# Performance work log

Measured on AMD Instinct MI355X. Metric: run time of the kernel, lower is better.

Reference implementation:

```python
import jax, jax.numpy as jnp
import numpy as np

ASPECT_RATIOS = jnp.array([0.5, 1.0, 2.0], dtype=jnp.float32)
SCALES = jnp.array([1.0, 2.0, 4.0, 8.0, 16.0], dtype=jnp.float32)
BASE_SIZE = 16
STRIDE = 16
NEG_OVERLAP = 0.3
POS_OVERLAP = 0.7
PADDING = 0.0
RPN_BATCH = 256
RPN_FG_FRACTION = 0.5


def _mkanchors(ws, hs, x_ctr, y_ctr):
    return jnp.stack([x_ctr - 0.5 * (ws - 1), y_ctr - 0.5 * (hs - 1),
                      x_ctr + 0.5 * (ws - 1), y_ctr + 0.5 * (hs - 1)], axis=-1)


def _base_anchors():
    w = h = float(BASE_SIZE)
    x_ctr = y_ctr = 0.5 * (BASE_SIZE - 1)
    size = w * h
    size_ratios = size / ASPECT_RATIOS
    ws = jnp.round(jnp.sqrt(size_ratios))
    hs = jnp.round(ws * ASPECT_RATIOS)
    ratio_anchors = _mkanchors(ws, hs, x_ctr, y_ctr)          # (R,4)
    rw = ratio_anchors[:, 2] - ratio_anchors[:, 0] + 1
    rh = ratio_anchors[:, 3] - ratio_anchors[:, 1] + 1
    rx = ratio_anchors[:, 0] + 0.5 * (rw - 1)
    ry = ratio_anchors[:, 1] + 0.5 * (rh - 1)
    ws2 = rw[:, None] * SCALES[None, :]                        # (R,S)
    hs2 = rh[:, None] * SCALES[None, :]
    anchors = _mkanchors(ws2, hs2, rx[:, None], ry[:, None])   # (R,S,4)
    return anchors.reshape(-1, 4)                              # (A=R*S,4)


def _shifted_anchors(r, c):
    base = _base_anchors()                                     # (A,4)
    sx = jnp.arange(c, dtype=jnp.float32) * STRIDE
    sy = jnp.arange(r, dtype=jnp.float32) * STRIDE
    SX, SY = jnp.meshgrid(sx, sy)                              # (r,c)
    shifts = jnp.stack([SX.ravel(), SY.ravel(), SX.ravel(), SY.ravel()], axis=1)
    return (shifts[:, None, :] + base[None, :, :]).reshape(-1, 4)  # (K=r*c*A,4)


def _iou(a, b):
    area_a = (a[:, 2] - a[:, 0] + 1) * (a[:, 3] - a[:, 1] + 1)
    area_b = (b[:, 2] - b[:, 0] + 1) * (b[:, 3] - b[:, 1] + 1)
    iw = jnp.minimum(a[:, None, 2], b[None, :, 2]) - jnp.maximum(a[:, None, 0], b[None, :, 0]) + 1
    ih = jnp.minimum(a[:, None, 3], b[None, :, 3]) - jnp.maximum(a[:, None, 1], b[None, :, 1]) + 1
    inter = jnp.maximum(iw, 0) * jnp.maximum(ih, 0)
    return inter / (area_a[:, None] + area_b[None, :] - inter)


def _bbox_transform(ex, gt):
    ew = ex[:, 2] - ex[:, 0] + 1.0
    eh = ex[:, 3] - ex[:, 1] + 1.0
    ecx = ex[:, 0] + 0.5 * ew
    ecy = ex[:, 1] + 0.5 * eh
    gw = gt[:, 2] - gt[:, 0] + 1.0
    gh = gt[:, 3] - gt[:, 1] + 1.0
    gcx = gt[:, 0] + 0.5 * gw
    gcy = gt[:, 1] + 0.5 * gh
    return jnp.stack([(gcx - ecx) / ew, (gcy - ecy) / eh,
                      jnp.log(gw / ew), jnp.log(gh / eh)], axis=1)


def reference(target_bounding_boxes, metadata, scores):
    meta = metadata[0]
    gt = target_bounding_boxes[0]                               # (G,4)
    r, c = scores.shape[1], scores.shape[2]
    anchors = _shifted_anchors(r, c)                            # (K,4)
    K = anchors.shape[0]
    h, w = meta[0], meta[1]

    # anchors fully inside the image (padding=0); outside anchors masked
    inside = ((anchors[:, 0] >= -PADDING) & (anchors[:, 1] >= -PADDING) &
              (anchors[:, 2] < w + PADDING) & (anchors[:, 3] < h + PADDING))

    clipped = jnp.stack([jnp.clip(anchors[:, 0], 0.0, w - 1),
                         jnp.clip(anchors[:, 1], 0.0, h - 1),
                         jnp.clip(anchors[:, 2], 0.0, w - 1),
                         jnp.clip(anchors[:, 3], 0.0, h - 1)], axis=1)

    overlaps = _iou(clipped, gt)                                # (K,G)
    overlaps = jnp.where(inside[:, None], overlaps, -1.0)       # ignore outside anchors
    argmax_overlaps = jnp.argmax(overlaps, axis=1)              # best gt per anchor
    max_overlaps = jnp.max(overlaps, axis=1)
    gt_argmax = jnp.argmax(overlaps, axis=0)                    # best anchor per gt

    labels = jnp.full((K,), -1.0, dtype=jnp.float32)
    labels = jnp.where(inside & (max_overlaps < NEG_OVERLAP), 0.0, labels)
    labels = labels.at[gt_argmax].set(1.0)                      # dedup handled by .set
    labels = jnp.where(inside & (max_overlaps >= POS_OVERLAP), 1.0, labels)
    labels = jnp.where(inside, labels, -1.0)                    # unmap fill=-1

    # deterministic subsampling (original shuffles randomly): keep first-by-index
    num_fg = int(RPN_FG_FRACTION * RPN_BATCH)
    pos = labels == 1.0
    pos_rank = jnp.cumsum(pos.astype(jnp.int32))
    labels = jnp.where(pos & (pos_rank > num_fg), -1.0, labels)
    num_pos = jnp.minimum(pos.sum(), num_fg)
    num_bg = RPN_BATCH - num_pos
    neg = labels == 0.0
    neg_rank = jnp.cumsum(neg.astype(jnp.int32))
    labels = jnp.where(neg & (neg_rank > num_bg), -1.0, labels)

    matched_gt = gt[argmax_overlaps]                            # (K,4) gather
    bbox_targets = _bbox_transform(clipped, matched_gt)
    bbox_targets = jnp.where(inside[:, None], bbox_targets, 0.0)  # unmap fill=0

    return anchors[None], bbox_targets[None], labels[None]


def setup_inputs() -> dict:
    key = jax.random.key(0)
    k1, k2 = jax.random.split(key)
    H = W = 1600
    G = 100
    r = c = H // STRIDE                                          # 100
    A = 15                                                       # 3 ratios * 5 scales
    xy = jax.random.uniform(k1, (G, 2), minval=0.0, maxval=1400.0)
    wh = jax.random.uniform(k2, (G, 2), minval=16.0, maxval=200.0)
    gt = jnp.concatenate([xy, xy + wh], axis=1)[None]            # (1,G,4)
    metadata = jnp.array([[float(H), float(W), 1.0]], dtype=jnp.float32)
    scores = jnp.zeros((1, r, c, A), dtype=jnp.float32)          # only shape is used
    return {"target_bounding_boxes": gt, "metadata": metadata, "scores": scores}
```

## Files before the change

### kernel.cpp

```cpp
#include <hip/hip_runtime.h>
#include <math.h>


#define NUM_A 15
#define NUM_FG 128
#define RPN_BATCH 256
#define BLOCK 256
#define MAXG 256
#define MAXNB 1024

#define EXT_X1 (-176.f)
#define EXT_X2 (191.f)
#define EXT_Y1 (-168.f)
#define EXT_Y2 (183.f)

__device__ __forceinline__ void base_anchor(int a, float& bx1, float& by1,
                                            float& bx2, float& by2) {
    const float RW[3] = {23.f, 16.f, 11.f};
    const float RH[3] = {12.f, 16.f, 22.f};
    int i = a / 5;
    int j = a - i * 5;
    float sc = (float)(1 << j);
    float w = RW[i] * sc;
    float h = RH[i] * sc;
    bx1 = 7.5f - 0.5f * (w - 1.f);
    by1 = 7.5f - 0.5f * (h - 1.f);
    bx2 = 7.5f + 0.5f * (w - 1.f);
    by2 = 7.5f + 0.5f * (h - 1.f);
}

__device__ __forceinline__ void anchor_coords(int k, int c, float& x1, float& y1,
                                              float& x2, float& y2) {
    int a = k % NUM_A;
    int p = k / NUM_A;
    int xi = p % c;
    int yi = p / c;
    float bx1, by1, bx2, by2;
    base_anchor(a, bx1, by1, bx2, by2);
    float sx = (float)xi * 16.f;
    float sy = (float)yi * 16.f;
    x1 = sx + bx1;  y1 = sy + by1;
    x2 = sx + bx2;  y2 = sy + by2;
}

__device__ __forceinline__ unsigned long long packvk(float v, int k) {
    unsigned u = __float_as_uint(v);
    u = (u & 0x80000000u) ? ~u : (u | 0x80000000u);
    return ((unsigned long long)u << 32) | (unsigned)(~k);
}

__global__ void __launch_bounds__(BLOCK) k_main(
        const float* __restrict__ gt, const float* __restrict__ meta,
        float* __restrict__ out_anch, float* __restrict__ out_bb,
        float* __restrict__ lab0, int* __restrict__ posc, int* __restrict__ negc,
        unsigned long long* __restrict__ bestg, int K, int c, int G) {
    __shared__ float4 s_gt[MAXG];
    __shared__ float4 s_gtc[MAXG];
    __shared__ int s_gidx[MAXG];
    __shared__ unsigned long long s_best[MAXG];
    __shared__ int s_nl;
    __shared__ int swp[4], swn[4];
    int tid = threadIdx.x;
    int lane = tid & 63, wid = tid >> 6;
    const float4* gtv = (const float4*)gt;

    float h = meta[0], w = meta[1];
    float wm1 = __fsub_rn(w, 1.f), hm1 = __fsub_rn(h, 1.f);

    int k0 = blockIdx.x * BLOCK;
    int k1 = min(k0 + BLOCK - 1, K - 1);
    int p0 = k0 / NUM_A, p1 = k1 / NUM_A;
    int y0 = p0 / c, y1 = p1 / c;
    int xm0, xm1;
    if (y0 == y1) { xm0 = p0 - y0 * c; xm1 = p1 - y1 * c; }
    else          { xm0 = 0;           xm1 = c - 1; }
    float bbx1 = fminf(fmaxf((float)(xm0 * 16) + EXT_X1, 0.f), wm1);
    float bbx2 = fminf(fmaxf((float)(xm1 * 16) + EXT_X2, 0.f), wm1);
    float bby1 = fminf(fmaxf((float)(y0 * 16) + EXT_Y1, 0.f), hm1);
    float bby2 = fminf(fmaxf((float)(y1 * 16) + EXT_Y2, 0.f), hm1);

    if (tid == 0) s_nl = 0;
    for (int g = tid; g < G; g += BLOCK) s_best[g] = 0ULL;
    __syncthreads();
    for (int g = tid; g < G; g += BLOCK) {
        float4 gb = gtv[g];
        s_gt[g] = gb;
        float ox = __fadd_rn(__fsub_rn(fminf(bbx2, gb.z), fmaxf(bbx1, gb.x)), 1.f);
        float oy = __fadd_rn(__fsub_rn(fminf(bby2, gb.w), fmaxf(bby1, gb.y)), 1.f);
        if (ox > 0.f && oy > 0.f) {
            int slot = atomicAdd(&s_nl, 1);
            s_gtc[slot] = gb;
            s_gidx[slot] = g;
        }
    }
    __syncthreads();
    int NL = s_nl;

    int k = blockIdx.x * BLOCK + tid;
    bool valid = (k < K);

    float x1, y1f, x2, y2f;
    anchor_coords(k, c, x1, y1f, x2, y2f);
    if (valid) ((float4*)out_anch)[k] = make_float4(x1, y1f, x2, y2f);
    bool inside = (x1 >= 0.f) && (y1f >= 0.f) && (x2 < w) && (y2f < h);
    bool act_anchor = valid && inside;

    float cx1 = fminf(fmaxf(x1, 0.f), wm1);
    float cy1 = fminf(fmaxf(y1f, 0.f), hm1);
    float cx2 = fminf(fmaxf(x2, 0.f), wm1);
    float cy2 = fminf(fmaxf(y2f, 0.f), hm1);
    float area_a = __fmul_rn(__fadd_rn(__fsub_rn(cx2, cx1), 1.f),
                             __fadd_rn(__fsub_rn(cy2, cy1), 1.f));

    float maxv = 0.f;
    int arg = 0;
    if (act_anchor) {
        for (int i = 0; i < NL; ++i) {
            float4 gb = s_gtc[i];
            int g = s_gidx[i];
            float gw = __fadd_rn(__fsub_rn(gb.z, gb.x), 1.f);
            float gh = __fadd_rn(__fsub_rn(gb.w, gb.y), 1.f);
            float areab = __fmul_rn(gw, gh);
            float iw = __fadd_rn(__fsub_rn(fminf(cx2, gb.z), fmaxf(cx1, gb.x)), 1.f);
            float ih = __fadd_rn(__fsub_rn(fminf(cy2, gb.w), fmaxf(cy1, gb.y)), 1.f);
            float inter = __fmul_rn(fmaxf(iw, 0.f), fmaxf(ih, 0.f));
            if (inter > 0.f) {
                float denom = __fsub_rn(__fadd_rn(area_a, areab), inter);
                float v = __fdiv_rn(inter, denom);
                atomicMax(&s_best[g], packvk(v, k));
                if (v > maxv || (v == maxv && g < arg)) { maxv = v; arg = g; }
            }
        }
    }
    __syncthreads();
    for (int g = tid; g < G; g += BLOCK)
        if (s_best[g] != 0ULL) atomicMax(&bestg[g], s_best[g]);

    float labf = -1.f;
    if (valid) {
        float t0 = 0.f, t1 = 0.f, t2 = 0.f, t3 = 0.f;
        if (inside) {
            labf = (maxv >= 0.7f) ? 1.f : (maxv < 0.3f ? 0.f : -1.f);
            float4 gb = s_gt[arg];
            float ew  = __fadd_rn(__fsub_rn(cx2, cx1), 1.f);
            float eh  = __fadd_rn(__fsub_rn(cy2, cy1), 1.f);
            float ecx = __fadd_rn(cx1, __fmul_rn(0.5f, ew));
            float ecy = __fadd_rn(cy1, __fmul_rn(0.5f, eh));
            float gw  = __fadd_rn(__fsub_rn(gb.z, gb.x), 1.f);
            float gh  = __fadd_rn(__fsub_rn(gb.w, gb.y), 1.f);
            float gcx = __fadd_rn(gb.x, __fmul_rn(0.5f, gw));
            float gcy = __fadd_rn(gb.y, __fmul_rn(0.5f, gh));
            t0 = __fdiv_rn(__fsub_rn(gcx, ecx), ew);
            t1 = __fdiv_rn(__fsub_rn(gcy, ecy), eh);
            t2 = logf(__fdiv_rn(gw, ew));
            t3 = logf(__fdiv_rn(gh, eh));
        }
        ((float4*)out_bb)[k] = make_float4(t0, t1, t2, t3);
        lab0[k] = labf;
    }

    bool pos = valid && (labf == 1.f);
    bool neg = valid && (labf == 0.f);
    unsigned long long bp = __ballot(pos ? 1 : 0);
    unsigned long long bn = __ballot(neg ? 1 : 0);
    if (lane == 0) { swp[wid] = __popcll(bp); swn[wid] = __popcll(bn); }
    __syncthreads();
    if (tid == 0) {
        posc[blockIdx.x] = swp[0] + swp[1] + swp[2] + swp[3];
        negc[blockIdx.x] = swn[0] + swn[1] + swn[2] + swn[3];
    }
}

__global__ void __launch_bounds__(BLOCK) k_finish(
        const float* __restrict__ lab0, float* __restrict__ out_lab,
        const int* __restrict__ posc, const int* __restrict__ negc,
        const unsigned long long* __restrict__ bestg, int K, int NB, int G) {
    __shared__ int s_p[MAXNB], s_n[MAXNB];
    __shared__ int s_cp[BLOCK], s_cn[BLOCK];
    __shared__ int s_k[MAXG];
    __shared__ unsigned char s_over[BLOCK];
    __shared__ int swp[4], swn[4];
    int tid = threadIdx.x;
    int lane = tid & 63, wid = tid >> 6;
    int base = tid * 4;

    int4 pv = ((const int4*)posc)[tid];
    int4 nv = ((const int4*)negc)[tid];
    if (base + 0 >= NB) pv.x = 0;  if (base + 1 >= NB) pv.y = 0;
    if (base + 2 >= NB) pv.z = 0;  if (base + 3 >= NB) pv.w = 0;
    if (base + 0 >= NB) nv.x = 0;  if (base + 1 >= NB) nv.y = 0;
    if (base + 2 >= NB) nv.z = 0;  if (base + 3 >= NB) nv.w = 0;
    ((int4*)s_p)[tid] = pv;
    ((int4*)s_n)[tid] = nv;

    s_over[tid] = 0;
    int kstar = -1;
    if (tid < G) {
        unsigned long long u = bestg[tid];
        if (u != 0ULL)
            kstar = (int)(~(unsigned)(u & 0xffffffffu));
    }
    if (tid < MAXG) s_k[tid] = kstar;
    __syncthreads();
    bool mine = (kstar >= 0);
    if (mine) {
        for (int j = 0; j < tid; ++j)
            if (s_k[j] == kstar) { mine = false; break; }
    }
    if (mine) {
        int b = kstar / BLOCK;
        float oldl = lab0[kstar];
        if (oldl != 1.f) {
            atomicAdd(&s_p[b], 1);
            if (oldl == 0.f) atomicAdd(&s_n[b], -1);
        }
        if (b == (int)blockIdx.x) s_over[kstar - b * BLOCK] = 1;
    }
    __syncthreads();

    int p0 = s_p[base], p1 = s_p[base + 1], p2 = s_p[base + 2], p3 = s_p[base + 3];
    int n0 = s_n[base], n1 = s_n[base + 1], n2 = s_n[base + 2], n3 = s_n[base + 3];
    int sump = p0 + p1 + p2 + p3, sumn = n0 + n1 + n2 + n3;
    s_cp[tid] = sump; s_cn[tid] = sumn;
    __syncthreads();
    int vp = sump, vn = sumn;
    for (int off = 1; off < BLOCK; off <<= 1) {
        int ap = 0, an = 0;
        if (tid >= off) { ap = s_cp[tid - off]; an = s_cn[tid - off]; }
        __syncthreads();
        vp += ap; vn += an;
        s_cp[tid] = vp; s_cn[tid] = vn;
        __syncthreads();
    }
    int ep = vp - sump, en = vn - sumn;
    s_p[base] = ep; ep += p0; s_p[base + 1] = ep; ep += p1;
    s_p[base + 2] = ep; ep += p2; s_p[base + 3] = ep;
    s_n[base] = en; en += n0; s_n[base + 1] = en; en += n1;
    s_n[base + 2] = en; en += n2; s_n[base + 3] = en;
    __syncthreads();
    int total_pos = s_cp[BLOCK - 1];
    int np = total_pos < NUM_FG ? total_pos : NUM_FG;
    int nbg = RPN_BATCH - np;

    int k = blockIdx.x * BLOCK + tid;
    bool valid = (k < K);
    float lv = -1.f;
    if (valid) lv = s_over[tid] ? 1.f : lab0[k];
    bool posf = valid && (lv == 1.f);
    bool negf = valid && (lv == 0.f);
    unsigned long long lm = (1ULL << lane) - 1ULL;
    unsigned long long bp2 = __ballot(posf ? 1 : 0);
    unsigned long long bn2 = __ballot(negf ? 1 : 0);
    if (lane == 0) { swp[wid] = __popcll(bp2); swn[wid] = __popcll(bn2); }
    __syncthreads();
    int poff = 0, noff = 0;
    for (int wv = 0; wv < wid; ++wv) { poff += swp[wv]; noff += swn[wv]; }
    int prank = s_p[blockIdx.x] + poff + __popcll(bp2 & lm) + 1;
    int nrank = s_n[blockIdx.x] + noff + __popcll(bn2 & lm) + 1;
    if (valid) {
        float outv = lv;
        if (posf && prank > NUM_FG) outv = -1.f;
        if (negf && nrank > nbg)    outv = -1.f;
        out_lab[k] = outv;
    }
}

extern "C" void kernel_launch(void* const* d_in, const int* in_sizes, int n_in,
                              void* d_out, int out_size, void* d_ws, size_t ws_size,
                              hipStream_t stream) {
    const float* gt   = (const float*)d_in[0];
    const float* meta = (const float*)d_in[1];
    int G  = in_sizes[0] / 4;
    int rc = in_sizes[2] / NUM_A;
    int c = 1;
    while ((long long)(c + 1) * (c + 1) <= (long long)rc) ++c;
    int K  = rc * NUM_A;
    int NB = (K + BLOCK - 1) / BLOCK;

    float* out      = (float*)d_out;
    float* out_anch = out;
    float* out_bb   = out + (size_t)4 * K;
    float* out_lab  = out + (size_t)8 * K;

    unsigned long long* bestg = (unsigned long long*)d_ws;
    int* posc  = (int*)(bestg + MAXG);
    int* negc  = posc + MAXNB;
    float* lab0 = (float*)(negc + MAXNB);

    hipMemsetAsync(bestg, 0, MAXG * sizeof(unsigned long long), stream);
    hipLaunchKernelGGL(k_main, dim3(NB), dim3(BLOCK), 0, stream,
                       gt, meta, out_anch, out_bb, lab0, posc, negc, bestg, K, c, G);
    hipLaunchKernelGGL(k_finish, dim3(NB), dim3(BLOCK), 0, stream,
                       lab0, out_lab, posc, negc, bestg, K, NB, G);
}
```

Before: 101.8 us.

## Replace global atomic best-anchor reduction with per-block candidate lists

Instead of each block doing global 64-bit atomicMax on a per-GT array (which needed a memset launch), each block writes its nonzero per-GT best records, tagged with the GT index, into its own slice of workspace. Each finish block then re-reduces all candidates in shared memory. This removes the memset and the global atomic contention, but every finish block redundantly scans all blocks' candidate lists. The anchor index is packed into 24 bits, which limits K.

```diff
diff --git a/kernel.cpp b/kernel.cpp
--- a/kernel.cpp
+++ b/kernel.cpp
@@ -8,6 +8,7 @@
 #define BLOCK 256
 #define MAXG 256
 #define MAXNB 1024
+#define SL 256
 
 #define EXT_X1 (-176.f)
 #define EXT_X2 (191.f)
@@ -43,22 +44,25 @@
     x2 = sx + bx2;  y2 = sy + by2;
 }
 
-__device__ __forceinline__ unsigned long long packvk(float v, int k) {
+__device__ __forceinline__ unsigned long long packvkg(float v, int k, int g) {
     unsigned u = __float_as_uint(v);
     u = (u & 0x80000000u) ? ~u : (u | 0x80000000u);
-    return ((unsigned long long)u << 32) | (unsigned)(~k);
+    unsigned nk = (~(unsigned)k) & 0xFFFFFFu;
+    return ((unsigned long long)u << 32) | ((unsigned long long)nk << 8)
+         | (unsigned)g;
 }
 
 __global__ void __launch_bounds__(BLOCK) k_main(
         const float* __restrict__ gt, const float* __restrict__ meta,
         float* __restrict__ out_anch, float* __restrict__ out_bb,
         float* __restrict__ lab0, int* __restrict__ posc, int* __restrict__ negc,
-        unsigned long long* __restrict__ bestg, int K, int c, int G) {
+        unsigned long long* __restrict__ cpk, int* __restrict__ ccnt,
+        int K, int c, int G) {
     __shared__ float4 s_gt[MAXG];
     __shared__ float4 s_gtc[MAXG];
     __shared__ int s_gidx[MAXG];
     __shared__ unsigned long long s_best[MAXG];
-    __shared__ int s_nl;
+    __shared__ int s_nl, s_nc;
     __shared__ int swp[4], swn[4];
     int tid = threadIdx.x;
     int lane = tid & 63, wid = tid >> 6;
@@ -79,7 +83,7 @@
     float bby1 = fminf(fmaxf((float)(y0 * 16) + EXT_Y1, 0.f), hm1);
     float bby2 = fminf(fmaxf((float)(y1 * 16) + EXT_Y2, 0.f), hm1);
 
-    if (tid == 0) s_nl = 0;
+    if (tid == 0) { s_nl = 0; s_nc = 0; }
     for (int g = tid; g < G; g += BLOCK) s_best[g] = 0ULL;
     __syncthreads();
     for (int g = tid; g < G; g += BLOCK) {
@@ -127,14 +131,19 @@
             if (inter > 0.f) {
                 float denom = __fsub_rn(__fadd_rn(area_a, areab), inter);
                 float v = __fdiv_rn(inter, denom);
-                atomicMax(&s_best[g], packvk(v, k));
+                atomicMax(&s_best[g], packvkg(v, k, g));
                 if (v > maxv || (v == maxv && g < arg)) { maxv = v; arg = g; }
             }
         }
     }
     __syncthreads();
-    for (int g = tid; g < G; g += BLOCK)
-        if (s_best[g] != 0ULL) atomicMax(&bestg[g], s_best[g]);
+    for (int g = tid; g < G; g += BLOCK) {
+        unsigned long long sb = s_best[g];
+        if (sb != 0ULL) {
+            int slot = atomicAdd(&s_nc, 1);
+            cpk[(size_t)blockIdx.x * SL + slot] = sb;
+        }
+    }
 
     float labf = -1.f;
     if (valid) {
@@ -168,16 +177,19 @@
     if (tid == 0) {
         posc[blockIdx.x] = swp[0] + swp[1] + swp[2] + swp[3];
         negc[blockIdx.x] = swn[0] + swn[1] + swn[2] + swn[3];
+        ccnt[blockIdx.x] = s_nc;
     }
 }
 
 __global__ void __launch_bounds__(BLOCK) k_finish(
         const float* __restrict__ lab0, float* __restrict__ out_lab,
         const int* __restrict__ posc, const int* __restrict__ negc,
-        const unsigned long long* __restrict__ bestg, int K, int NB, int G) {
-    __shared__ int s_p[MAXNB], s_n[MAXNB];
+        const unsigned long long* __restrict__ cpk, const int* __restrict__ ccnt,
+        int K, int NB, int G) {
+    __shared__ int s_p[MAXNB], s_n[MAXNB], s_ccnt[MAXNB];
     __shared__ int s_cp[BLOCK], s_cn[BLOCK];
     __shared__ int s_k[MAXG];
+    __shared__ unsigned long long s_best[MAXG];
     __shared__ unsigned char s_over[BLOCK];
     __shared__ int swp[4], swn[4];
     int tid = threadIdx.x;
@@ -186,19 +198,33 @@
 
     int4 pv = ((const int4*)posc)[tid];
     int4 nv = ((const int4*)negc)[tid];
+    int4 cv = ((const int4*)ccnt)[tid];
     if (base + 0 >= NB) pv.x = 0;  if (base + 1 >= NB) pv.y = 0;
     if (base + 2 >= NB) pv.z = 0;  if (base + 3 >= NB) pv.w = 0;
     if (base + 0 >= NB) nv.x = 0;  if (base + 1 >= NB) nv.y = 0;
     if (base + 2 >= NB) nv.z = 0;  if (base + 3 >= NB) nv.w = 0;
     ((int4*)s_p)[tid] = pv;
     ((int4*)s_n)[tid] = nv;
-
+    ((int4*)s_ccnt)[tid] = cv;
     s_over[tid] = 0;
+    if (tid < MAXG) s_best[tid] = 0ULL;
+    __syncthreads();
+
+    for (int b = tid; b < NB; b += BLOCK) {
+        int cnt = s_ccnt[b];
+        const unsigned long long* rp = cpk + (size_t)b * SL;
+        for (int i = 0; i < cnt; ++i) {
+            unsigned long long rec = rp[i];
+            atomicMax(&s_best[rec & 0xFFu], rec);
+        }
+    }
+    __syncthreads();
+
     int kstar = -1;
     if (tid < G) {
-        unsigned long long u = bestg[tid];
+        unsigned long long u = s_best[tid];
         if (u != 0ULL)
-            kstar = (int)(~(unsigned)(u & 0xffffffffu));
+            kstar = 0xFFFFFF ^ (int)((u >> 8) & 0xFFFFFFu);
     }
     if (tid < MAXG) s_k[tid] = kstar;
     __syncthreads();
@@ -282,14 +308,15 @@
     float* out_bb   = out + (size_t)4 * K;
     float* out_lab  = out + (size_t)8 * K;
 
-    unsigned long long* bestg = (unsigned long long*)d_ws;
-    int* posc  = (int*)(bestg + MAXG);
+    unsigned long long* cpk = (unsigned long long*)d_ws;
+    int* posc  = (int*)(cpk + (size_t)MAXNB * SL);
     int* negc  = posc + MAXNB;
-    float* lab0 = (float*)(negc + MAXNB);
-
-    hipMemsetAsync(bestg, 0, MAXG * sizeof(unsigned long long), stream);
+    int* ccnt  = negc + MAXNB;
+    float* lab0 = (float*)(ccnt + MAXNB);
+
     hipLaunchKernelGGL(k_main, dim3(NB), dim3(BLOCK), 0, stream,
-                       gt, meta, out_anch, out_bb, lab0, posc, negc, bestg, K, c, G);
+                       gt, meta, out_anch, out_bb, lab0, posc, negc, cpk, ccnt,
+                       K, c, G);
     hipLaunchKernelGGL(k_finish, dim3(NB), dim3(BLOCK), 0, stream,
-                       lab0, out_lab, posc, negc, bestg, K, NB, G);
-}
+                       lab0, out_lab, posc, negc, cpk, ccnt, K, NB, G);
+}
```

New measurement: 103.2 us. No clear change (+1.4%).

## Replace label finish pass with bitmask-based single-block sparse fixup

Applied to the files above, without the earlier changes.

The main kernel now writes -1 to every label and stores per-wave positive/negative ballot bitmasks instead of an intermediate label array and per-block counts. A single 1024-thread fixup kernel scans the bitmask popcounts, applies the best-anchor-per-gt overrides, and writes only the labels that survive subsampling (up to 128 positives and the negative budget). This drops the full second pass over K labels, the lab0 buffer traffic and a grid-wide kernel, at the cost of a serial single-block tail with per-thread bit-walking loops. The fixup assumes NB <= 1024 and that BLOCK equals 256 for its shift arithmetic.

```diff
diff --git a/kernel.cpp b/kernel.cpp
--- a/kernel.cpp
+++ b/kernel.cpp
@@ -8,6 +8,7 @@
 #define BLOCK 256
 #define MAXG 256
 #define MAXNB 1024
+#define FIXT 1024
 
 #define EXT_X1 (-176.f)
 #define EXT_X2 (191.f)
@@ -52,14 +53,14 @@
 __global__ void __launch_bounds__(BLOCK) k_main(
         const float* __restrict__ gt, const float* __restrict__ meta,
         float* __restrict__ out_anch, float* __restrict__ out_bb,
-        float* __restrict__ lab0, int* __restrict__ posc, int* __restrict__ negc,
+        float* __restrict__ out_lab,
+        unsigned long long* __restrict__ pbm, unsigned long long* __restrict__ nbm,
         unsigned long long* __restrict__ bestg, int K, int c, int G) {
     __shared__ float4 s_gt[MAXG];
     __shared__ float4 s_gtc[MAXG];
     __shared__ int s_gidx[MAXG];
     __shared__ unsigned long long s_best[MAXG];
     __shared__ int s_nl;
-    __shared__ int swp[4], swn[4];
     int tid = threadIdx.x;
     int lane = tid & 63, wid = tid >> 6;
     const float4* gtv = (const float4*)gt;
@@ -156,112 +157,112 @@
             t3 = logf(__fdiv_rn(gh, eh));
         }
         ((float4*)out_bb)[k] = make_float4(t0, t1, t2, t3);
-        lab0[k] = labf;
+        out_lab[k] = -1.f;
     }
 
     bool pos = valid && (labf == 1.f);
     bool neg = valid && (labf == 0.f);
     unsigned long long bp = __ballot(pos ? 1 : 0);
     unsigned long long bn = __ballot(neg ? 1 : 0);
-    if (lane == 0) { swp[wid] = __popcll(bp); swn[wid] = __popcll(bn); }
-    __syncthreads();
-    if (tid == 0) {
-        posc[blockIdx.x] = swp[0] + swp[1] + swp[2] + swp[3];
-        negc[blockIdx.x] = swn[0] + swn[1] + swn[2] + swn[3];
-    }
-}
-
-__global__ void __launch_bounds__(BLOCK) k_finish(
-        const float* __restrict__ lab0, float* __restrict__ out_lab,
-        const int* __restrict__ posc, const int* __restrict__ negc,
+    if (lane == 0) {
+        pbm[blockIdx.x * 4 + wid] = bp;
+        nbm[blockIdx.x * 4 + wid] = bn;
+    }
+}
+
+__global__ void __launch_bounds__(FIXT) k_fix(
+        float* __restrict__ out_lab,
+        const unsigned long long* __restrict__ pbm,
+        const unsigned long long* __restrict__ nbm,
         const unsigned long long* __restrict__ bestg, int K, int NB, int G) {
-    __shared__ int s_p[MAXNB], s_n[MAXNB];
-    __shared__ int s_cp[BLOCK], s_cn[BLOCK];
+    __shared__ int s_p[FIXT], s_n[FIXT];
     __shared__ int s_k[MAXG];
-    __shared__ unsigned char s_over[BLOCK];
-    __shared__ int swp[4], swn[4];
-    int tid = threadIdx.x;
-    int lane = tid & 63, wid = tid >> 6;
-    int base = tid * 4;
-
-    int4 pv = ((const int4*)posc)[tid];
-    int4 nv = ((const int4*)negc)[tid];
-    if (base + 0 >= NB) pv.x = 0;  if (base + 1 >= NB) pv.y = 0;
-    if (base + 2 >= NB) pv.z = 0;  if (base + 3 >= NB) pv.w = 0;
-    if (base + 0 >= NB) nv.x = 0;  if (base + 1 >= NB) nv.y = 0;
-    if (base + 2 >= NB) nv.z = 0;  if (base + 3 >= NB) nv.w = 0;
-    ((int4*)s_p)[tid] = pv;
-    ((int4*)s_n)[tid] = nv;
-
-    s_over[tid] = 0;
+    __shared__ unsigned long long cmask[MAXNB][4];
+    int t = threadIdx.x;
+
+    cmask[t][0] = 0ULL; cmask[t][1] = 0ULL;
+    cmask[t][2] = 0ULL; cmask[t][3] = 0ULL;
+
+    int cp = 0, cn = 0;
+    if (t < NB) {
+        const unsigned long long* pp = pbm + 4 * t;
+        const unsigned long long* nn = nbm + 4 * t;
+        cp = __popcll(pp[0]) + __popcll(pp[1]) + __popcll(pp[2]) + __popcll(pp[3]);
+        cn = __popcll(nn[0]) + __popcll(nn[1]) + __popcll(nn[2]) + __popcll(nn[3]);
+    }
+    s_p[t] = cp;
+    s_n[t] = cn;
+
     int kstar = -1;
-    if (tid < G) {
-        unsigned long long u = bestg[tid];
+    if (t < G) {
+        unsigned long long u = bestg[t];
         if (u != 0ULL)
             kstar = (int)(~(unsigned)(u & 0xffffffffu));
     }
-    if (tid < MAXG) s_k[tid] = kstar;
+    if (t < MAXG) s_k[t] = kstar;
     __syncthreads();
     bool mine = (kstar >= 0);
     if (mine) {
-        for (int j = 0; j < tid; ++j)
+        for (int j = 0; j < t; ++j)
             if (s_k[j] == kstar) { mine = false; break; }
     }
     if (mine) {
-        int b = kstar / BLOCK;
-        float oldl = lab0[kstar];
-        if (oldl != 1.f) {
+        int b = kstar >> 8;
+        int bit = kstar & 255;
+        unsigned long long msk = 1ULL << (bit & 63);
+        unsigned long long pw = pbm[b * 4 + (bit >> 6)];
+        unsigned long long nw = nbm[b * 4 + (bit >> 6)];
+        bool was1 = (pw & msk) != 0ULL;
+        bool was0 = (nw & msk) != 0ULL;
+        if (!was1) {
             atomicAdd(&s_p[b], 1);
-            if (oldl == 0.f) atomicAdd(&s_n[b], -1);
-        }
-        if (b == (int)blockIdx.x) s_over[kstar - b * BLOCK] = 1;
-    }
-    __syncthreads();
-
-    int p0 = s_p[base], p1 = s_p[base + 1], p2 = s_p[base + 2], p3 = s_p[base + 3];
-    int n0 = s_n[base], n1 = s_n[base + 1], n2 = s_n[base + 2], n3 = s_n[base + 3];
-    int sump = p0 + p1 + p2 + p3, sumn = n0 + n1 + n2 + n3;
-    s_cp[tid] = sump; s_cn[tid] = sumn;
-    __syncthreads();
-    int vp = sump, vn = sumn;
-    for (int off = 1; off < BLOCK; off <<= 1) {
+            if (was0) atomicAdd(&s_n[b], -1);
+        }
+        atomicOr(&cmask[b][bit >> 6], msk);
+    }
+    __syncthreads();
+
+    int op = s_p[t], on = s_n[t];
+    int vp = op, vn = on;
+    for (int off = 1; off < FIXT; off <<= 1) {
         int ap = 0, an = 0;
-        if (tid >= off) { ap = s_cp[tid - off]; an = s_cn[tid - off]; }
+        if (t >= off) { ap = s_p[t - off]; an = s_n[t - off]; }
         __syncthreads();
         vp += ap; vn += an;
-        s_cp[tid] = vp; s_cn[tid] = vn;
+        s_p[t] = vp; s_n[t] = vn;
         __syncthreads();
     }
-    int ep = vp - sump, en = vn - sumn;
-    s_p[base] = ep; ep += p0; s_p[base + 1] = ep; ep += p1;
-    s_p[base + 2] = ep; ep += p2; s_p[base + 3] = ep;
-    s_n[base] = en; en += n0; s_n[base + 1] = en; en += n1;
-    s_n[base + 2] = en; en += n2; s_n[base + 3] = en;
-    __syncthreads();
-    int total_pos = s_cp[BLOCK - 1];
+    int total_pos = s_p[FIXT - 1];
     int np = total_pos < NUM_FG ? total_pos : NUM_FG;
     int nbg = RPN_BATCH - np;
-
-    int k = blockIdx.x * BLOCK + tid;
-    bool valid = (k < K);
-    float lv = -1.f;
-    if (valid) lv = s_over[tid] ? 1.f : lab0[k];
-    bool posf = valid && (lv == 1.f);
-    bool negf = valid && (lv == 0.f);
-    unsigned long long lm = (1ULL << lane) - 1ULL;
-    unsigned long long bp2 = __ballot(posf ? 1 : 0);
-    unsigned long long bn2 = __ballot(negf ? 1 : 0);
-    if (lane == 0) { swp[wid] = __popcll(bp2); swn[wid] = __popcll(bn2); }
-    __syncthreads();
-    int poff = 0, noff = 0;
-    for (int wv = 0; wv < wid; ++wv) { poff += swp[wv]; noff += swn[wv]; }
-    int prank = s_p[blockIdx.x] + poff + __popcll(bp2 & lm) + 1;
-    int nrank = s_n[blockIdx.x] + noff + __popcll(bn2 & lm) + 1;
-    if (valid) {
-        float outv = lv;
-        if (posf && prank > NUM_FG) outv = -1.f;
-        if (negf && nrank > nbg)    outv = -1.f;
-        out_lab[k] = outv;
+    int ep = vp - op, en = vn - on;
+
+    if (t < NB) {
+        int base_k = t * BLOCK;
+        if (ep < NUM_FG && op > 0) {
+            int rank = ep;
+            for (int wd = 0; wd < 4 && rank < NUM_FG; ++wd) {
+                unsigned long long m = pbm[t * 4 + wd] | cmask[t][wd];
+                while (m != 0ULL && rank < NUM_FG) {
+                    int bit = __builtin_ctzll(m);
+                    m &= m - 1ULL;
+                    ++rank;
+                    out_lab[base_k + wd * 64 + bit] = 1.0f;
+                }
+            }
+        }
+        if (en < nbg && on > 0) {
+            int rank = en;
+            for (int wd = 0; wd < 4 && rank < nbg; ++wd) {
+                unsigned long long m = nbm[t * 4 + wd] & ~cmask[t][wd];
+                while (m != 0ULL && rank < nbg) {
+                    int bit = __builtin_ctzll(m);
+                    m &= m - 1ULL;
+                    ++rank;
+                    out_lab[base_k + wd * 64 + bit] = 0.0f;
+                }
+            }
+        }
     }
 }
 
@@ -283,13 +284,12 @@
     float* out_lab  = out + (size_t)8 * K;
 
     unsigned long long* bestg = (unsigned long long*)d_ws;
-    int* posc  = (int*)(bestg + MAXG);
-    int* negc  = posc + MAXNB;
-    float* lab0 = (float*)(negc + MAXNB);
-
-    hipMemsetAsync(bestg, 0, MAXG * sizeof(unsigned long long), stream);
+    unsigned long long* pbm   = bestg + MAXG;
+    unsigned long long* nbm   = pbm + (size_t)MAXNB * 4;
+
+    hipMemsetAsync(bestg, 0, (size_t)G * sizeof(unsigned long long), stream);
     hipLaunchKernelGGL(k_main, dim3(NB), dim3(BLOCK), 0, stream,
-                       gt, meta, out_anch, out_bb, lab0, posc, negc, bestg, K, c, G);
-    hipLaunchKernelGGL(k_finish, dim3(NB), dim3(BLOCK), 0, stream,
-                       lab0, out_lab, posc, negc, bestg, K, NB, G);
-}
+                       gt, meta, out_anch, out_bb, out_lab, pbm, nbm, bestg, K, c, G);
+    hipLaunchKernelGGL(k_fix, dim3(1), dim3(FIXT), 0, stream,
+                       out_lab, pbm, nbm, bestg, K, NB, G);
+}
```

After: 105.0 us. +3.2%, slower.
